# Kernel optimization log

Hardware: AMD Instinct MI355X
Metric: run time of the kernel (lower is better)

The kernel has to match this reference:

```python
import jax, jax.numpy as jnp
import numpy as np

N_NODES = 50000
N_EDGES = 1600000
N_GRAPHS = 512
HID = 64


def _mlp_params(key, din, dout, scale=0.1):
    k1, k2, k3 = jax.random.split(key, 3)
    return (
        jax.random.normal(k1, (din, HID), jnp.float32) * scale, jnp.zeros((HID,), jnp.float32),
        jax.random.normal(k2, (HID, HID), jnp.float32) * scale, jnp.zeros((HID,), jnp.float32),
        jax.random.normal(k3, (HID, dout), jnp.float32) * scale, jnp.zeros((dout,), jnp.float32),
    )


def _mlp(x, w1, b1, w2, b2, w3, b3, out_act=None):
    h = jax.nn.relu(x @ w1 + b1)
    h = jax.nn.relu(h @ w2 + b2)
    o = h @ w3 + b3
    return o if out_act is None else out_act(o)


def setup_inputs() -> dict:
    key = jax.random.key(0)
    ks = jax.random.split(key, 8)
    nf = jax.random.normal(ks[0], (N_NODES, 1), jnp.float32)
    ef = jax.random.normal(ks[1], (N_EDGES, 1), jnp.float32)
    src = jax.random.randint(ks[2], (N_EDGES,), 0, N_NODES)
    dst = jax.random.randint(ks[3], (N_EDGES,), 0, N_NODES)
    graph_id = jnp.sort(jax.random.randint(ks[4], (N_NODES,), 0, N_GRAPHS))
    e_w1, e_b1, e_w2, e_b2, e_w3, e_b3 = _mlp_params(ks[5], 3, 1)   # edge model: [src_nf, dst_nf, ef] -> msg
    n_w1, n_b1, n_w2, n_b2, n_w3, n_b3 = _mlp_params(ks[6], 2, 1)   # node model: [nf, agg] -> unf
    m_w1, m_b1, m_w2, m_b2, m_w3, m_b3 = _mlp_params(ks[7], 1, 1)   # node-wise MLP with Sigmoid out_act
    return dict(nf=nf, ef=ef, src=src, dst=dst, graph_id=graph_id,
                e_w1=e_w1, e_b1=e_b1, e_w2=e_w2, e_b2=e_b2, e_w3=e_w3, e_b3=e_b3,
                n_w1=n_w1, n_b1=n_b1, n_w2=n_w2, n_b2=n_b2, n_w3=n_w3, n_b3=n_b3,
                m_w1=m_w1, m_b1=m_b1, m_w2=m_w2, m_b2=m_b2, m_w3=m_w3, m_b3=m_b3)


def reference(nf, ef, src, dst, graph_id,
              e_w1, e_b1, e_w2, e_b2, e_w3, e_b3,
              n_w1, n_b1, n_w2, n_b2, n_w3, n_b3,
              m_w1, m_b1, m_w2, m_b2, m_w3, m_b3):
    # MPNN layer: message on edges, sum-aggregate to dst nodes, node update
    em_in = jnp.concatenate([nf[src], nf[dst], ef], axis=-1)          # [E, 3]
    msg = _mlp(em_in, e_w1, e_b1, e_w2, e_b2, e_w3, e_b3)             # [E, 1]
    agg = jax.ops.segment_sum(msg, dst, num_segments=N_NODES)        # [N, 1]
    unf = _mlp(jnp.concatenate([nf, agg], axis=-1),
               n_w1, n_b1, n_w2, n_b2, n_w3, n_b3)                    # [N, 1]
    # node-wise MLP with Sigmoid output activation
    node_out = _mlp(unf, m_w1, m_b1, m_w2, m_b2, m_w3, m_b3,
                    out_act=jax.nn.sigmoid)                           # [N, 1]
    # sum readout per graph, then final sigmoid
    rd = jax.ops.segment_sum(node_out, graph_id, num_segments=N_GRAPHS)  # [G, 1]
    return jax.nn.sigmoid(rd)
```

## Files before the change

### kernel.cpp

```cpp
#include <hip/hip_runtime.h>
#include <math.h>

#define HID 64
#define BKT_SHIFT 13
#define BKT_RANGE 8192
#define CCHUNK 32

typedef __attribute__((ext_vector_type(8))) short short8;
typedef __attribute__((ext_vector_type(4))) float f32x4;
typedef unsigned long long ull;

union FragU {
    uint4 q;
    short8 v;
    uint32_t u[4];
};

__device__ __forceinline__ uint32_t cvt_pk_bf16(float lo, float hi) {
    uint32_t r;
    asm("v_cvt_pk_bf16_f32 %0, %1, %2" : "=v"(r) : "v"(lo), "v"(hi));
    return r;
}

__global__ __launch_bounds__(256, 2) void edge_mfma8_kernel(
    const float* __restrict__ nf, const float* __restrict__ ef,
    const int* __restrict__ src, const int* __restrict__ dst,
    const float* __restrict__ w1, const float* __restrict__ b1,
    const float* __restrict__ w2, const float* __restrict__ b2,
    const float* __restrict__ w3, const float* __restrict__ b3,
    uint2* __restrict__ recs, ull* __restrict__ offs,
    float* __restrict__ aggFb, int E, int B, int nbatch, int mode)
{
    __shared__ uint2 tile[4][4][16][16];

    const int tid  = threadIdx.x;
    const int lane = tid & 63;
    const int wid  = tid >> 6;
    const int g    = lane >> 4;
    const int eL   = lane & 15;

    FragU af1[4];
#pragma unroll
    for (int t = 0; t < 4; ++t) {
        int j = t * 16 + eL;
        uint32_t u0 = cvt_pk_bf16(w1[j], w1[HID + j]);
        uint32_t u1 = cvt_pk_bf16(w1[2 * HID + j], b1[j]);
        af1[t].u[0] = (g == 0) ? u0 : 0u;
        af1[t].u[1] = (g == 0) ? u1 : 0u;
        af1[t].u[2] = 0u; af1[t].u[3] = 0u;
    }
    FragU af2[4][2];
#pragma unroll
    for (int t = 0; t < 4; ++t)
#pragma unroll
        for (int h = 0; h < 2; ++h)
#pragma unroll
            for (int e2 = 0; e2 < 4; ++e2) {
                int k0 = h * 32 + g * 8 + 2 * e2;
                int j  = t * 16 + eL;
                af2[t][h].u[e2] = cvt_pk_bf16(w2[k0 * HID + j], w2[(k0 + 1) * HID + j]);
            }
    f32x4 b2v4[4], w3v4[4];
#pragma unroll
    for (int t = 0; t < 4; ++t) {
        int j = t * 16 + g * 4;
        b2v4[t] = *(const f32x4*)&b2[j];
        w3v4[t] = *(const f32x4*)&w3[j];
    }
    const float b3c = b3[0];

    int bi   = blockIdx.x;
    if (bi >= nbatch) return;
    int eidx = bi * 256 + tid;
    int ei   = eidx < E ? eidx : E - 1;
    int dcur = dst[ei];
    float a  = nf[src[ei]];
    float b  = nf[dcur];
    float c  = ef[ei];
    uint32_t pkab = cvt_pk_bf16(a, b);
    uint32_t pkc1 = cvt_pk_bf16(c, 1.0f);

    for (;;) {
        const int nbi   = bi + gridDim.x;
        const bool hn   = nbi < nbatch;
        const int neidx = hn ? nbi * 256 + tid : eidx;
        const int nei   = neidx < E ? neidx : E - 1;
        const int ns    = src[nei];
        const int nd    = dst[nei];
        const float ncf = ef[nei];

#pragma unroll
        for (int s = 0; s < 4; ++s) {
            int sel = s * 16 + eL;
            uint32_t u0 = (uint32_t)__shfl((int)pkab, sel);
            uint32_t u1 = (uint32_t)__shfl((int)pkc1, sel);
            FragU bin;
            bin.u[0] = (g == 0) ? u0 : 0u;
            bin.u[1] = (g == 0) ? u1 : 0u;
            bin.u[2] = 0u; bin.u[3] = 0u;
#pragma unroll
            for (int t = 0; t < 4; ++t) {
                f32x4 h4 = __builtin_amdgcn_mfma_f32_16x16x32_bf16(
                    af1[t].v, bin.v, (f32x4){0.f, 0.f, 0.f, 0.f}, 0, 0, 0);
                uint32_t p0 = cvt_pk_bf16(fmaxf(h4[0], 0.f), fmaxf(h4[1], 0.f));
                uint32_t p1 = cvt_pk_bf16(fmaxf(h4[2], 0.f), fmaxf(h4[3], 0.f));
                tile[wid][s][eL][(4 * t + g) ^ ((eL & 7) << 1)] = make_uint2(p0, p1);
            }
        }

        const float na = nf[ns];
        const float nb = nf[nd];

        float mymsg = 0.f;
#pragma unroll
        for (int s = 0; s < 4; ++s) {
            const uint4* row = (const uint4*)&tile[wid][s][eL][0];
            FragU bf0, bf1;
            bf0.q = row[(g)     ^ (eL & 7)];
            bf1.q = row[(4 + g) ^ (eL & 7)];

            float q0, q1, q2, q3;
            {
                f32x4 ac = __builtin_amdgcn_mfma_f32_16x16x32_bf16(af2[0][0].v, bf0.v, b2v4[0], 0, 0, 0);
                ac = __builtin_amdgcn_mfma_f32_16x16x32_bf16(af2[0][1].v, bf1.v, ac, 0, 0, 0);
                q0 = fmaxf(ac[0], 0.f) * w3v4[0][0];
                q0 = fmaf(fmaxf(ac[1], 0.f), w3v4[0][1], q0);
                q0 = fmaf(fmaxf(ac[2], 0.f), w3v4[0][2], q0);
                q0 = fmaf(fmaxf(ac[3], 0.f), w3v4[0][3], q0);
            }
            {
                f32x4 ac = __builtin_amdgcn_mfma_f32_16x16x32_bf16(af2[1][0].v, bf0.v, b2v4[1], 0, 0, 0);
                ac = __builtin_amdgcn_mfma_f32_16x16x32_bf16(af2[1][1].v, bf1.v, ac, 0, 0, 0);
                q1 = fmaxf(ac[0], 0.f) * w3v4[1][0];
                q1 = fmaf(fmaxf(ac[1], 0.f), w3v4[1][1], q1);
                q1 = fmaf(fmaxf(ac[2], 0.f), w3v4[1][2], q1);
                q1 = fmaf(fmaxf(ac[3], 0.f), w3v4[1][3], q1);
            }
            {
                f32x4 ac = __builtin_amdgcn_mfma_f32_16x16x32_bf16(af2[2][0].v, bf0.v, b2v4[2], 0, 0, 0);
                ac = __builtin_amdgcn_mfma_f32_16x16x32_bf16(af2[2][1].v, bf1.v, ac, 0, 0, 0);
                q2 = fmaxf(ac[0], 0.f) * w3v4[2][0];
                q2 = fmaf(fmaxf(ac[1], 0.f), w3v4[2][1], q2);
                q2 = fmaf(fmaxf(ac[2], 0.f), w3v4[2][2], q2);
                q2 = fmaf(fmaxf(ac[3], 0.f), w3v4[2][3], q2);
            }
            {
                f32x4 ac = __builtin_amdgcn_mfma_f32_16x16x32_bf16(af2[3][0].v, bf0.v, b2v4[3], 0, 0, 0);
                ac = __builtin_amdgcn_mfma_f32_16x16x32_bf16(af2[3][1].v, bf1.v, ac, 0, 0, 0);
                q3 = fmaxf(ac[0], 0.f) * w3v4[3][0];
                q3 = fmaf(fmaxf(ac[1], 0.f), w3v4[3][1], q3);
                q3 = fmaf(fmaxf(ac[2], 0.f), w3v4[3][2], q3);
                q3 = fmaf(fmaxf(ac[3], 0.f), w3v4[3][3], q3);
            }
            float p = (q0 + q1) + (q2 + q3);
            p += __shfl_xor(p, 16);
            p += __shfl_xor(p, 32);
            if (s == g) mymsg = p + b3c;
        }

        const bool valid = eidx < E;

        if (mode == 1) {
            if (valid) atomicAdd(&aggFb[dcur], mymsg);
        } else {
            const int bkt = dcur >> BKT_SHIFT;
            const ull lt = (1ull << lane) - 1;
            int myslot = 0;
            int off = 0;
            uint32_t pack_lo = 0, pack_hi = 0;
            for (int bb = 0; bb < B; ++bb) {
                if (bb < 4) pack_lo |= (uint32_t)off << (8 * bb);
                else        pack_hi |= (uint32_t)off << (8 * (bb - 4));
                ull m = __ballot(valid && bkt == bb);
                if (valid && bkt == bb) myslot = off + (int)__popcll(m & lt);
                off += (int)__popcll(m);
            }
            pack_hi |= (uint32_t)off << 24;

            const size_t wgl = (size_t)bi * 4 + wid;
            if (valid) recs[wgl * 64 + myslot] = make_uint2((uint32_t)dcur, __float_as_uint(mymsg));
            if (lane == 0) offs[wgl] = ((ull)pack_hi << 32) | (ull)pack_lo;
        }

        if (!hn) break;
        bi = nbi; eidx = neidx;
        pkab = cvt_pk_bf16(na, nb);
        pkc1 = cvt_pk_bf16(ncf, 1.0f);
        dcur = nd;
    }
}

__global__ __launch_bounds__(256) void bucket_accum_kernel(
    const uint2* __restrict__ recs, const ull* __restrict__ offs,
    float* __restrict__ partial, float* __restrict__ rd, unsigned* __restrict__ ctr,
    int G, int NW, int B)
{
    __shared__ float acc[BKT_RANGE];

    const int b = blockIdx.x / CCHUNK;
    const int c = blockIdx.x % CCHUNK;

    if (blockIdx.x == 0) {
        for (int i = threadIdx.x; i < G; i += 256) rd[i] = 0.f;
        if (threadIdx.x == 0) *ctr = 0u;
    }

    for (int i = threadIdx.x; i < BKT_RANGE; i += 256) acc[i] = 0.f;
    __syncthreads();

    const int wpc = (NW + CCHUNK - 1) / CCHUNK;
    const int w0 = c * wpc;
    const int w1 = (w0 + wpc < NW) ? w0 + wpc : NW;
    const int nb = b + 1;
    const int base_node = b << BKT_SHIFT;

    for (int w = w0 + threadIdx.x; w < w1; w += 256) {
        ull ov = offs[w];
        uint32_t lo = (uint32_t)ov, hi = (uint32_t)(ov >> 32);
        int ob = (int)(((b  < 4) ? (lo >> (8 * b))  : (hi >> (8 * (b  - 4)))) & 0xFF);
        int oe = (int)(((nb < 4) ? (lo >> (8 * nb)) : (hi >> (8 * (nb - 4)))) & 0xFF);
        const uint2* rb = recs + (size_t)w * 64;
        for (int r = ob; r < oe; ++r) {
            uint2 rec = rb[r];
            atomicAdd(&acc[(int)rec.x - base_node], __uint_as_float(rec.y));
        }
    }
    __syncthreads();

    float* pb = partial + ((size_t)b * CCHUNK + c) * BKT_RANGE;
    for (int i = threadIdx.x; i < BKT_RANGE; i += 256) pb[i] = acc[i];
}

__global__ __launch_bounds__(256, 2) void node_mfma5_kernel(
    const float* __restrict__ nf, const float* __restrict__ partial,
    const float* __restrict__ aggFb, int nplanes,
    const int* __restrict__ gid,
    const float* __restrict__ nw1, const float* __restrict__ nb1,
    const float* __restrict__ nw2, const float* __restrict__ nb2,
    const float* __restrict__ nw3, const float* __restrict__ nb3,
    const float* __restrict__ mw1, const float* __restrict__ mb1,
    const float* __restrict__ mw2, const float* __restrict__ mb2,
    const float* __restrict__ mw3, const float* __restrict__ mb3,
    float* __restrict__ rd, float* __restrict__ outp, unsigned* __restrict__ ctr,
    int N, int G)
{
    __shared__ uint2 tile[4][4][16][16];
    __shared__ int lastflag;

    const int tid  = threadIdx.x;
    const int lane = tid & 63;
    const int wid  = tid >> 6;
    const int g    = lane >> 4;
    const int eL   = lane & 15;

    const int idx = blockIdx.x * 256 + tid;
    const int i   = idx < N ? idx : N - 1;
    const float x0 = nf[i];
    const int   gg = gid[i];

    float x1;
    if (nplanes == 1) {
        x1 = aggFb[i];
    } else {
        int bb = i >> BKT_SHIFT, nl = i & (BKT_RANGE - 1);
        const float* p = partial + (size_t)bb * CCHUNK * BKT_RANGE + nl;
        x1 = 0.f;
#pragma unroll 8
        for (int c = 0; c < CCHUNK; ++c) x1 += p[(size_t)c * BKT_RANGE];
    }

    float myunf = 0.f, o = 0.f;

    {
        FragU af1[4], af2[4][2];
        f32x4 b2v4[4], w3v4[4];
#pragma unroll
        for (int t = 0; t < 4; ++t) {
            int j = t * 16 + eL;
            uint32_t u0 = cvt_pk_bf16(nw1[j], nw1[HID + j]);
            uint32_t u1 = cvt_pk_bf16(nb1[j], 0.f);
            af1[t].u[0] = (g == 0) ? u0 : 0u;
            af1[t].u[1] = (g == 0) ? u1 : 0u;
            af1[t].u[2] = 0u; af1[t].u[3] = 0u;
#pragma unroll
            for (int h = 0; h < 2; ++h)
#pragma unroll
                for (int e2 = 0; e2 < 4; ++e2) {
                    int k0 = h * 32 + g * 8 + 2 * e2;
                    af2[t][h].u[e2] = cvt_pk_bf16(nw2[k0 * HID + j], nw2[(k0 + 1) * HID + j]);
                }
            int j4 = t * 16 + g * 4;
            b2v4[t] = *(const f32x4*)&nb2[j4];
            w3v4[t] = *(const f32x4*)&nw3[j4];
        }
        uint32_t pk01 = cvt_pk_bf16(x0, x1);
        uint32_t pkb  = cvt_pk_bf16(1.0f, 0.f);

#pragma unroll
        for (int s = 0; s < 4; ++s) {
            int sel = s * 16 + eL;
            uint32_t u0 = (uint32_t)__shfl((int)pk01, sel);
            FragU bin;
            bin.u[0] = (g == 0) ? u0 : 0u;
            bin.u[1] = (g == 0) ? pkb : 0u;
            bin.u[2] = 0u; bin.u[3] = 0u;
#pragma unroll
            for (int t = 0; t < 4; ++t) {
                f32x4 h4 = __builtin_amdgcn_mfma_f32_16x16x32_bf16(
                    af1[t].v, bin.v, (f32x4){0.f, 0.f, 0.f, 0.f}, 0, 0, 0);
                uint32_t p0 = cvt_pk_bf16(fmaxf(h4[0], 0.f), fmaxf(h4[1], 0.f));
                uint32_t p1 = cvt_pk_bf16(fmaxf(h4[2], 0.f), fmaxf(h4[3], 0.f));
                tile[wid][s][eL][(4 * t + g) ^ ((eL & 7) << 1)] = make_uint2(p0, p1);
            }
        }
#pragma unroll
        for (int s = 0; s < 4; ++s) {
            const uint4* row = (const uint4*)&tile[wid][s][eL][0];
            FragU bf0, bf1;
            bf0.q = row[(g)     ^ (eL & 7)];
            bf1.q = row[(4 + g) ^ (eL & 7)];
            float p = 0.f;
#pragma unroll
            for (int t = 0; t < 4; ++t) {
                f32x4 ac = __builtin_amdgcn_mfma_f32_16x16x32_bf16(af2[t][0].v, bf0.v, b2v4[t], 0, 0, 0);
                ac = __builtin_amdgcn_mfma_f32_16x16x32_bf16(af2[t][1].v, bf1.v, ac, 0, 0, 0);
                p = fmaf(fmaxf(ac[0], 0.f), w3v4[t][0], p);
                p = fmaf(fmaxf(ac[1], 0.f), w3v4[t][1], p);
                p = fmaf(fmaxf(ac[2], 0.f), w3v4[t][2], p);
                p = fmaf(fmaxf(ac[3], 0.f), w3v4[t][3], p);
            }
            p += __shfl_xor(p, 16);
            p += __shfl_xor(p, 32);
            if (s == g) myunf = p + nb3[0];
        }
    }

    {
        FragU af1[4], af2[4][2];
        f32x4 b2v4[4], w3v4[4];
#pragma unroll
        for (int t = 0; t < 4; ++t) {
            int j = t * 16 + eL;
            uint32_t u0 = cvt_pk_bf16(mw1[j], mb1[j]);
            af1[t].u[0] = (g == 0) ? u0 : 0u;
            af1[t].u[1] = 0u; af1[t].u[2] = 0u; af1[t].u[3] = 0u;
#pragma unroll
            for (int h = 0; h < 2; ++h)
#pragma unroll
                for (int e2 = 0; e2 < 4; ++e2) {
                    int k0 = h * 32 + g * 8 + 2 * e2;
                    af2[t][h].u[e2] = cvt_pk_bf16(mw2[k0 * HID + j], mw2[(k0 + 1) * HID + j]);
                }
            int j4 = t * 16 + g * 4;
            b2v4[t] = *(const f32x4*)&mb2[j4];
            w3v4[t] = *(const f32x4*)&mw3[j4];
        }

#pragma unroll
        for (int s = 0; s < 4; ++s) {
            float uv = __shfl(myunf, s * 16 + eL);
            FragU bin;
            bin.u[0] = (g == 0) ? cvt_pk_bf16(uv, 1.0f) : 0u;
            bin.u[1] = 0u; bin.u[2] = 0u; bin.u[3] = 0u;
#pragma unroll
            for (int t = 0; t < 4; ++t) {
                f32x4 h4 = __builtin_amdgcn_mfma_f32_16x16x32_bf16(
                    af1[t].v, bin.v, (f32x4){0.f, 0.f, 0.f, 0.f}, 0, 0, 0);
                uint32_t p0 = cvt_pk_bf16(fmaxf(h4[0], 0.f), fmaxf(h4[1], 0.f));
                uint32_t p1 = cvt_pk_bf16(fmaxf(h4[2], 0.f), fmaxf(h4[3], 0.f));
                tile[wid][s][eL][(4 * t + g) ^ ((eL & 7) << 1)] = make_uint2(p0, p1);
            }
        }
#pragma unroll
        for (int s = 0; s < 4; ++s) {
            const uint4* row = (const uint4*)&tile[wid][s][eL][0];
            FragU bf0, bf1;
            bf0.q = row[(g)     ^ (eL & 7)];
            bf1.q = row[(4 + g) ^ (eL & 7)];
            float p = 0.f;
#pragma unroll
            for (int t = 0; t < 4; ++t) {
                f32x4 ac = __builtin_amdgcn_mfma_f32_16x16x32_bf16(af2[t][0].v, bf0.v, b2v4[t], 0, 0, 0);
                ac = __builtin_amdgcn_mfma_f32_16x16x32_bf16(af2[t][1].v, bf1.v, ac, 0, 0, 0);
                p = fmaf(fmaxf(ac[0], 0.f), w3v4[t][0], p);
                p = fmaf(fmaxf(ac[1], 0.f), w3v4[t][1], p);
                p = fmaf(fmaxf(ac[2], 0.f), w3v4[t][2], p);
                p = fmaf(fmaxf(ac[3], 0.f), w3v4[t][3], p);
            }
            p += __shfl_xor(p, 16);
            p += __shfl_xor(p, 32);
            if (s == g) o = p + mb3[0];
        }
    }

    const float node_out = 1.0f / (1.0f + expf(-o));

    {
        const bool ok = idx < N;
        float v = ok ? node_out : 0.0f;
        int ggv = gg;
#pragma unroll
        for (int d = 1; d < 64; d <<= 1) {
            float vup = __shfl_up(v, d);
            int   gup = __shfl_up(ggv, d);
            if (lane >= d && gup == ggv) v += vup;
        }
        int gdn = __shfl_down(ggv, 1);
        bool tail = (lane == 63) || (gdn != ggv);
        if (tail)
            atomicAdd(&rd[ggv], v);
    }

    if (ctr) {
        if (tid == 0) {
            __threadfence();
            unsigned v = atomicAdd(ctr, 1u);
            lastflag = (v == (unsigned)(gridDim.x - 1)) ? 1 : 0;
        }
        __syncthreads();
        if (lastflag) {
            __threadfence();
            for (int q = tid; q < G; q += 256)
                outp[q] = 1.0f / (1.0f + expf(-rd[q]));
        }
    }
}

__global__ void readout_kernel(const float* __restrict__ rd,
                               float* __restrict__ out, int G)
{
    int g = blockIdx.x * blockDim.x + threadIdx.x;
    if (g < G) out[g] = 1.0f / (1.0f + expf(-rd[g]));
}

extern "C" void kernel_launch(void* const* d_in, const int* in_sizes, int n_in,
                              void* d_out, int out_size, void* d_ws, size_t ws_size,
                              hipStream_t stream)
{
    const float* nf  = (const float*)d_in[0];
    const float* ef  = (const float*)d_in[1];
    const int*   src = (const int*)  d_in[2];
    const int*   dst = (const int*)  d_in[3];
    const int*   gid = (const int*)  d_in[4];

    const float* e_w1 = (const float*)d_in[5];
    const float* e_b1 = (const float*)d_in[6];
    const float* e_w2 = (const float*)d_in[7];
    const float* e_b2 = (const float*)d_in[8];
    const float* e_w3 = (const float*)d_in[9];
    const float* e_b3 = (const float*)d_in[10];

    const float* n_w1 = (const float*)d_in[11];
    const float* n_b1 = (const float*)d_in[12];
    const float* n_w2 = (const float*)d_in[13];
    const float* n_b2 = (const float*)d_in[14];
    const float* n_w3 = (const float*)d_in[15];
    const float* n_b3 = (const float*)d_in[16];

    const float* m_w1 = (const float*)d_in[17];
    const float* m_b1 = (const float*)d_in[18];
    const float* m_w2 = (const float*)d_in[19];
    const float* m_b2 = (const float*)d_in[20];
    const float* m_w3 = (const float*)d_in[21];
    const float* m_b3 = (const float*)d_in[22];

    const int N = in_sizes[0];
    const int E = in_sizes[2];
    const int G = out_size;

    const int nbatch = (E + 255) / 256;
    const int NW = (E + 63) / 64;
    const int B  = (N + BKT_RANGE - 1) / BKT_RANGE;

    size_t recs_b = (size_t)NW * 64 * sizeof(uint2);
    size_t offs_b = (size_t)NW * sizeof(ull);
    size_t part_b = (size_t)B * CCHUNK * BKT_RANGE * sizeof(float);
    size_t need   = recs_b + offs_b + part_b + (size_t)G * sizeof(float) + 64;
    bool bucketok = (B <= 8) && (need <= ws_size);

    char* wp = (char*)d_ws;
    float* out = (float*)d_out;

    int egrid = nbatch < 1024 ? nbatch : 1024;

    if (bucketok) {
        uint2*    recs    = (uint2*)wp;
        ull*      offs    = (ull*)(wp + recs_b);
        float*    partial = (float*)(wp + recs_b + offs_b);
        float*    rd      = (float*)(wp + recs_b + offs_b + part_b);
        unsigned* ctr     = (unsigned*)(wp + recs_b + offs_b + part_b + (size_t)G * sizeof(float));

        edge_mfma8_kernel<<<egrid, 256, 0, stream>>>(
            nf, ef, src, dst, e_w1, e_b1, e_w2, e_b2, e_w3, e_b3,
            recs, offs, nullptr, E, B, nbatch, 0);

        bucket_accum_kernel<<<B * CCHUNK, 256, 0, stream>>>(
            recs, offs, partial, rd, ctr, G, NW, B);

        node_mfma5_kernel<<<(N + 255) / 256, 256, 0, stream>>>(
            nf, partial, nullptr, CCHUNK, gid,
            n_w1, n_b1, n_w2, n_b2, n_w3, n_b3,
            m_w1, m_b1, m_w2, m_b2, m_w3, m_b3,
            rd, out, ctr, N, G);
    } else {
        float* agg = (float*)wp;
        float* rd  = agg + N;

        hipMemsetAsync(agg, 0, ((size_t)N + G) * sizeof(float), stream);

        edge_mfma8_kernel<<<egrid, 256, 0, stream>>>(
            nf, ef, src, dst, e_w1, e_b1, e_w2, e_b2, e_w3, e_b3,
            nullptr, nullptr, agg, E, B, nbatch, 1);

        node_mfma5_kernel<<<(N + 255) / 256, 256, 0, stream>>>(
            nf, nullptr, agg, 1, gid,
            n_w1, n_b1, n_w2, n_b2, n_w3, n_b3,
            m_w1, m_b1, m_w2, m_b2, m_w3, m_b3,
            rd, out, nullptr, N, G);

        readout_kernel<<<(G + 255) / 256, 256, 0, stream>>>(rd, out, G);
    }
}
```

Baseline: 71.94 us.

## Drop per-wave bucket sorting; bucket kernel scans all edge records and filters

The edge kernel no longer ballots records into per-wave bucket slots with packed offsets. It writes each (dst, msg) record at its edge index. The bucket accumulation kernel now has every bucket's blocks scan the full record array in paired 16-byte loads and keep only records whose destination falls in their bucket. This removes the ballot loop and offset metadata but multiplies record reads by the bucket count (7 here). The node kernel is also moved to 128-thread blocks.

```diff
diff --git a/kernel.cpp b/kernel.cpp
--- a/kernel.cpp
+++ b/kernel.cpp
@@ -22,14 +22,14 @@
     return r;
 }
 
-__global__ __launch_bounds__(256, 2) void edge_mfma8_kernel(
+__global__ __launch_bounds__(256, 2) void edge_mfma9_kernel(
     const float* __restrict__ nf, const float* __restrict__ ef,
     const int* __restrict__ src, const int* __restrict__ dst,
     const float* __restrict__ w1, const float* __restrict__ b1,
     const float* __restrict__ w2, const float* __restrict__ b2,
     const float* __restrict__ w3, const float* __restrict__ b3,
-    uint2* __restrict__ recs, ull* __restrict__ offs,
-    float* __restrict__ aggFb, int E, int B, int nbatch, int mode)
+    uint2* __restrict__ recs,
+    float* __restrict__ aggFb, int E, int nbatch, int mode)
 {
     __shared__ uint2 tile[4][4][16][16];
 
@@ -163,23 +163,7 @@
         if (mode == 1) {
             if (valid) atomicAdd(&aggFb[dcur], mymsg);
         } else {
-            const int bkt = dcur >> BKT_SHIFT;
-            const ull lt = (1ull << lane) - 1;
-            int myslot = 0;
-            int off = 0;
-            uint32_t pack_lo = 0, pack_hi = 0;
-            for (int bb = 0; bb < B; ++bb) {
-                if (bb < 4) pack_lo |= (uint32_t)off << (8 * bb);
-                else        pack_hi |= (uint32_t)off << (8 * (bb - 4));
-                ull m = __ballot(valid && bkt == bb);
-                if (valid && bkt == bb) myslot = off + (int)__popcll(m & lt);
-                off += (int)__popcll(m);
-            }
-            pack_hi |= (uint32_t)off << 24;
-
-            const size_t wgl = (size_t)bi * 4 + wid;
-            if (valid) recs[wgl * 64 + myslot] = make_uint2((uint32_t)dcur, __float_as_uint(mymsg));
-            if (lane == 0) offs[wgl] = ((ull)pack_hi << 32) | (ull)pack_lo;
+            if (valid) recs[eidx] = make_uint2((uint32_t)dcur, __float_as_uint(mymsg));
         }
 
         if (!hn) break;
@@ -190,10 +174,10 @@
     }
 }
 
-__global__ __launch_bounds__(256) void bucket_accum_kernel(
-    const uint2* __restrict__ recs, const ull* __restrict__ offs,
-    float* __restrict__ partial, float* __restrict__ rd, unsigned* __restrict__ ctr,
-    int G, int NW, int B)
+__global__ __launch_bounds__(256) void bucket_accum2_kernel(
+    const uint2* __restrict__ recs, float* __restrict__ partial,
+    float* __restrict__ rd, unsigned* __restrict__ ctr,
+    int G, int E, int B)
 {
     __shared__ float acc[BKT_RANGE];
 
@@ -208,21 +192,21 @@
     for (int i = threadIdx.x; i < BKT_RANGE; i += 256) acc[i] = 0.f;
     __syncthreads();
 
-    const int wpc = (NW + CCHUNK - 1) / CCHUNK;
-    const int w0 = c * wpc;
-    const int w1 = (w0 + wpc < NW) ? w0 + wpc : NW;
-    const int nb = b + 1;
+    const int epc = (((E + CCHUNK - 1) / CCHUNK) + 1) & ~1;
+    const int e0 = c * epc;
+    const int e1 = (e0 + epc < E) ? e0 + epc : E;
     const int base_node = b << BKT_SHIFT;
 
-    for (int w = w0 + threadIdx.x; w < w1; w += 256) {
-        ull ov = offs[w];
-        uint32_t lo = (uint32_t)ov, hi = (uint32_t)(ov >> 32);
-        int ob = (int)(((b  < 4) ? (lo >> (8 * b))  : (hi >> (8 * (b  - 4)))) & 0xFF);
-        int oe = (int)(((nb < 4) ? (lo >> (8 * nb)) : (hi >> (8 * (nb - 4)))) & 0xFF);
-        const uint2* rb = recs + (size_t)w * 64;
-        for (int r = ob; r < oe; ++r) {
-            uint2 rec = rb[r];
-            atomicAdd(&acc[(int)rec.x - base_node], __uint_as_float(rec.y));
+    for (int e = e0 + threadIdx.x * 2; e < e1; e += 512) {
+        if (e + 1 < e1) {
+            uint4 two = *reinterpret_cast<const uint4*>(&recs[e]);
+            int d0 = (int)two.x, d1 = (int)two.z;
+            if ((d0 >> BKT_SHIFT) == b) atomicAdd(&acc[d0 - base_node], __uint_as_float(two.y));
+            if ((d1 >> BKT_SHIFT) == b) atomicAdd(&acc[d1 - base_node], __uint_as_float(two.w));
+        } else {
+            uint2 r = recs[e];
+            int d0 = (int)r.x;
+            if ((d0 >> BKT_SHIFT) == b) atomicAdd(&acc[d0 - base_node], __uint_as_float(r.y));
         }
     }
     __syncthreads();
@@ -231,7 +215,7 @@
     for (int i = threadIdx.x; i < BKT_RANGE; i += 256) pb[i] = acc[i];
 }
 
-__global__ __launch_bounds__(256, 2) void node_mfma5_kernel(
+__global__ __launch_bounds__(128, 2) void node_mfma6_kernel(
     const float* __restrict__ nf, const float* __restrict__ partial,
     const float* __restrict__ aggFb, int nplanes,
     const int* __restrict__ gid,
@@ -244,7 +228,7 @@
     float* __restrict__ rd, float* __restrict__ outp, unsigned* __restrict__ ctr,
     int N, int G)
 {
-    __shared__ uint2 tile[4][4][16][16];
+    __shared__ uint2 tile[2][4][16][16];
     __shared__ int lastflag;
 
     const int tid  = threadIdx.x;
@@ -253,7 +237,7 @@
     const int g    = lane >> 4;
     const int eL   = lane & 15;
 
-    const int idx = blockIdx.x * 256 + tid;
+    const int idx = blockIdx.x * 128 + tid;
     const int i   = idx < N ? idx : N - 1;
     const float x0 = nf[i];
     const int   gg = gid[i];
@@ -420,7 +404,7 @@
         __syncthreads();
         if (lastflag) {
             __threadfence();
-            for (int q = tid; q < G; q += 256)
+            for (int q = tid; q < G; q += 128)
                 outp[q] = 1.0f / (1.0f + expf(-rd[q]));
         }
     }
@@ -469,13 +453,11 @@
     const int G = out_size;
 
     const int nbatch = (E + 255) / 256;
-    const int NW = (E + 63) / 64;
     const int B  = (N + BKT_RANGE - 1) / BKT_RANGE;
 
-    size_t recs_b = (size_t)NW * 64 * sizeof(uint2);
-    size_t offs_b = (size_t)NW * sizeof(ull);
+    size_t recs_b = (size_t)E * sizeof(uint2);
     size_t part_b = (size_t)B * CCHUNK * BKT_RANGE * sizeof(float);
-    size_t need   = recs_b + offs_b + part_b + (size_t)G * sizeof(float) + 64;
+    size_t need   = recs_b + part_b + (size_t)G * sizeof(float) + 64;
     bool bucketok = (B <= 8) && (need <= ws_size);
 
     char* wp = (char*)d_ws;
@@ -485,19 +467,18 @@
 
     if (bucketok) {
         uint2*    recs    = (uint2*)wp;
-        ull*      offs    = (ull*)(wp + recs_b);
-        float*    partial = (float*)(wp + recs_b + offs_b);
-        float*    rd      = (float*)(wp + recs_b + offs_b + part_b);
-        unsigned* ctr     = (unsigned*)(wp + recs_b + offs_b + part_b + (size_t)G * sizeof(float));
-
-        edge_mfma8_kernel<<<egrid, 256, 0, stream>>>(
+        float*    partial = (float*)(wp + recs_b);
+        float*    rd      = (float*)(wp + recs_b + part_b);
+        unsigned* ctr     = (unsigned*)(wp + recs_b + part_b + (size_t)G * sizeof(float));
+
+        edge_mfma9_kernel<<<egrid, 256, 0, stream>>>(
             nf, ef, src, dst, e_w1, e_b1, e_w2, e_b2, e_w3, e_b3,
-            recs, offs, nullptr, E, B, nbatch, 0);
-
-        bucket_accum_kernel<<<B * CCHUNK, 256, 0, stream>>>(
-            recs, offs, partial, rd, ctr, G, NW, B);
-
-        node_mfma5_kernel<<<(N + 255) / 256, 256, 0, stream>>>(
+            recs, nullptr, E, nbatch, 0);
+
+        bucket_accum2_kernel<<<B * CCHUNK, 256, 0, stream>>>(
+            recs, partial, rd, ctr, G, E, B);
+
+        node_mfma6_kernel<<<(N + 127) / 128, 128, 0, stream>>>(
             nf, partial, nullptr, CCHUNK, gid,
             n_w1, n_b1, n_w2, n_b2, n_w3, n_b3,
             m_w1, m_b1, m_w2, m_b2, m_w3, m_b3,
@@ -508,11 +489,11 @@
 
         hipMemsetAsync(agg, 0, ((size_t)N + G) * sizeof(float), stream);
 
-        edge_mfma8_kernel<<<egrid, 256, 0, stream>>>(
+        edge_mfma9_kernel<<<egrid, 256, 0, stream>>>(
             nf, ef, src, dst, e_w1, e_b1, e_w2, e_b2, e_w3, e_b3,
-            nullptr, nullptr, agg, E, B, nbatch, 1);
-
-        node_mfma5_kernel<<<(N + 255) / 256, 256, 0, stream>>>(
+            nullptr, agg, E, nbatch, 1);
+
+        node_mfma6_kernel<<<(N + 127) / 128, 128, 0, stream>>>(
             nf, nullptr, agg, 1, gid,
             n_w1, n_b1, n_w2, n_b2, n_w3, n_b3,
             m_w1, m_b1, m_w2, m_b2, m_w3, m_b3,
```

Measured after the change: 98.91 us. 1.37x slower.

## Interleave two edge batches per loop iteration in edge MLP kernel

Applied to the files above, without the earlier changes.

The edge kernel now carries two 256-edge batches (A and B, one grid-stride apart) through each loop iteration. The layer-1 and layer-2 MFMA work and the LDS tile staging of both batches are interleaved, and the next pair's gathers are prefetched midway. The aim is more independent work in flight to hide MFMA, LDS and gather latency, and half as many loop iterations. The cost is higher register pressure under the (256, 2) launch bound, and possible imbalance when a block has an odd number of batches.

```diff
diff --git a/kernel.cpp b/kernel.cpp
--- a/kernel.cpp
+++ b/kernel.cpp
@@ -22,7 +22,7 @@
     return r;
 }
 
-__global__ __launch_bounds__(256, 2) void edge_mfma8_kernel(
+__global__ __launch_bounds__(256, 2) void edge_dual_kernel(
     const float* __restrict__ nf, const float* __restrict__ ef,
     const int* __restrict__ src, const int* __restrict__ dst,
     const float* __restrict__ w1, const float* __restrict__ b1,
@@ -31,7 +31,7 @@
     uint2* __restrict__ recs, ull* __restrict__ offs,
     float* __restrict__ aggFb, int E, int B, int nbatch, int mode)
 {
-    __shared__ uint2 tile[4][4][16][16];
+    __shared__ uint2 tile[4][2][2][16][16];
 
     const int tid  = threadIdx.x;
     const int lane = tid & 63;
@@ -69,124 +69,169 @@
     }
     const float b3c = b3[0];
 
-    int bi   = blockIdx.x;
-    if (bi >= nbatch) return;
-    int eidx = bi * 256 + tid;
-    int ei   = eidx < E ? eidx : E - 1;
-    int dcur = dst[ei];
-    float a  = nf[src[ei]];
-    float b  = nf[dcur];
-    float c  = ef[ei];
-    uint32_t pkab = cvt_pk_bf16(a, b);
-    uint32_t pkc1 = cvt_pk_bf16(c, 1.0f);
+    auto L1SET = [&](uint32_t ab, uint32_t c1, int s, uint2 (*tl)[16]) {
+        int sel = s * 16 + eL;
+        uint32_t u0 = (uint32_t)__shfl((int)ab, sel);
+        uint32_t u1 = (uint32_t)__shfl((int)c1, sel);
+        FragU bin;
+        bin.u[0] = (g == 0) ? u0 : 0u;
+        bin.u[1] = (g == 0) ? u1 : 0u;
+        bin.u[2] = 0u; bin.u[3] = 0u;
+#pragma unroll
+        for (int t = 0; t < 4; ++t) {
+            f32x4 h4 = __builtin_amdgcn_mfma_f32_16x16x32_bf16(
+                af1[t].v, bin.v, (f32x4){0.f, 0.f, 0.f, 0.f}, 0, 0, 0);
+            uint32_t p0 = cvt_pk_bf16(fmaxf(h4[0], 0.f), fmaxf(h4[1], 0.f));
+            uint32_t p1 = cvt_pk_bf16(fmaxf(h4[2], 0.f), fmaxf(h4[3], 0.f));
+            tl[eL][(4 * t + g) ^ ((eL & 7) << 1)] = make_uint2(p0, p1);
+        }
+    };
+    auto L2SET = [&](uint2 (*tl)[16]) -> float {
+        const uint4* row = (const uint4*)&tl[eL][0];
+        FragU bf0, bf1;
+        bf0.q = row[(g)     ^ (eL & 7)];
+        bf1.q = row[(4 + g) ^ (eL & 7)];
+        float q0, q1, q2, q3;
+        {
+            f32x4 ac = __builtin_amdgcn_mfma_f32_16x16x32_bf16(af2[0][0].v, bf0.v, b2v4[0], 0, 0, 0);
+            ac = __builtin_amdgcn_mfma_f32_16x16x32_bf16(af2[0][1].v, bf1.v, ac, 0, 0, 0);
+            q0 = fmaxf(ac[0], 0.f) * w3v4[0][0];
+            q0 = fmaf(fmaxf(ac[1], 0.f), w3v4[0][1], q0);
+            q0 = fmaf(fmaxf(ac[2], 0.f), w3v4[0][2], q0);
+            q0 = fmaf(fmaxf(ac[3], 0.f), w3v4[0][3], q0);
+        }
+        {
+            f32x4 ac = __builtin_amdgcn_mfma_f32_16x16x32_bf16(af2[1][0].v, bf0.v, b2v4[1], 0, 0, 0);
+            ac = __builtin_amdgcn_mfma_f32_16x16x32_bf16(af2[1][1].v, bf1.v, ac, 0, 0, 0);
+            q1 = fmaxf(ac[0], 0.f) * w3v4[1][0];
+            q1 = fmaf(fmaxf(ac[1], 0.f), w3v4[1][1], q1);
+            q1 = fmaf(fmaxf(ac[2], 0.f), w3v4[1][2], q1);
+            q1 = fmaf(fmaxf(ac[3], 0.f), w3v4[1][3], q1);
+        }
+        {
+            f32x4 ac = __builtin_amdgcn_mfma_f32_16x16x32_bf16(af2[2][0].v, bf0.v, b2v4[2], 0, 0, 0);
+            ac = __builtin_amdgcn_mfma_f32_16x16x32_bf16(af2[2][1].v, bf1.v, ac, 0, 0, 0);
+            q2 = fmaxf(ac[0], 0.f) * w3v4[2][0];
+            q2 = fmaf(fmaxf(ac[1], 0.f), w3v4[2][1], q2);
+            q2 = fmaf(fmaxf(ac[2], 0.f), w3v4[2][2], q2);
+            q2 = fmaf(fmaxf(ac[3], 0.f), w3v4[2][3], q2);
+        }
+        {
+            f32x4 ac = __builtin_amdgcn_mfma_f32_16x16x32_bf16(af2[3][0].v, bf0.v, b2v4[3], 0, 0, 0);
+            ac = __builtin_amdgcn_mfma_f32_16x16x32_bf16(af2[3][1].v, bf1.v, ac, 0, 0, 0);
+            q3 = fmaxf(ac[0], 0.f) * w3v4[3][0];
+            q3 = fmaf(fmaxf(ac[1], 0.f), w3v4[3][1], q3);
+            q3 = fmaf(fmaxf(ac[2], 0.f), w3v4[3][2], q3);
+            q3 = fmaf(fmaxf(ac[3], 0.f), w3v4[3][3], q3);
+        }
+        float p = (q0 + q1) + (q2 + q3);
+        p += __shfl_xor(p, 16);
+        p += __shfl_xor(p, 32);
+        return p;
+    };
+    auto APPEND = [&](int bb_i, int eix, int dc, float msg) {
+        const bool valid = eix < E;
+        const int bkt = dc >> BKT_SHIFT;
+        const ull lt = (1ull << lane) - 1;
+        int myslot = 0;
+        int off = 0;
+        uint32_t plo = 0, phi = 0;
+        for (int bb = 0; bb < B; ++bb) {
+            if (bb < 4) plo |= (uint32_t)off << (8 * bb);
+            else        phi |= (uint32_t)off << (8 * (bb - 4));
+            ull m = __ballot(valid && bkt == bb);
+            if (valid && bkt == bb) myslot = off + (int)__popcll(m & lt);
+            off += (int)__popcll(m);
+        }
+        phi |= (uint32_t)off << 24;
+        const size_t wgl = (size_t)bb_i * 4 + wid;
+        if (valid) recs[wgl * 64 + myslot] = make_uint2((uint32_t)dc, __float_as_uint(msg));
+        if (lane == 0) offs[wgl] = ((ull)phi << 32) | (ull)plo;
+    };
+
+    const int gsz = gridDim.x;
+    int biA = blockIdx.x;
+    if (biA >= nbatch) return;
+
+    int eixA = biA * 256 + tid;
+    int eiA  = eixA < E ? eixA : E - 1;
+    int dcA  = dst[eiA];
+    float aA = nf[src[eiA]];
+    float bA = nf[dcA];
+    float cA = ef[eiA];
+    uint32_t abA = cvt_pk_bf16(aA, bA);
+    uint32_t c1A = cvt_pk_bf16(cA, 1.0f);
+
+    int  biB  = biA + gsz;
+    bool hasB = biB < nbatch;
+    int eixB = hasB ? biB * 256 + tid : eixA;
+    int eiB  = eixB < E ? eixB : E - 1;
+    int dcB  = dst[eiB];
+    float aB = nf[src[eiB]];
+    float bB = nf[dcB];
+    float cB = ef[eiB];
+    uint32_t abB = cvt_pk_bf16(aB, bB);
+    uint32_t c1B = cvt_pk_bf16(cB, 1.0f);
 
     for (;;) {
-        const int nbi   = bi + gridDim.x;
-        const bool hn   = nbi < nbatch;
-        const int neidx = hn ? nbi * 256 + tid : eidx;
-        const int nei   = neidx < E ? neidx : E - 1;
-        const int ns    = src[nei];
-        const int nd    = dst[nei];
-        const float ncf = ef[nei];
-
-#pragma unroll
-        for (int s = 0; s < 4; ++s) {
-            int sel = s * 16 + eL;
-            uint32_t u0 = (uint32_t)__shfl((int)pkab, sel);
-            uint32_t u1 = (uint32_t)__shfl((int)pkc1, sel);
-            FragU bin;
-            bin.u[0] = (g == 0) ? u0 : 0u;
-            bin.u[1] = (g == 0) ? u1 : 0u;
-            bin.u[2] = 0u; bin.u[3] = 0u;
-#pragma unroll
-            for (int t = 0; t < 4; ++t) {
-                f32x4 h4 = __builtin_amdgcn_mfma_f32_16x16x32_bf16(
-                    af1[t].v, bin.v, (f32x4){0.f, 0.f, 0.f, 0.f}, 0, 0, 0);
-                uint32_t p0 = cvt_pk_bf16(fmaxf(h4[0], 0.f), fmaxf(h4[1], 0.f));
-                uint32_t p1 = cvt_pk_bf16(fmaxf(h4[2], 0.f), fmaxf(h4[3], 0.f));
-                tile[wid][s][eL][(4 * t + g) ^ ((eL & 7) << 1)] = make_uint2(p0, p1);
-            }
-        }
-
-        const float na = nf[ns];
-        const float nb = nf[nd];
-
-        float mymsg = 0.f;
-#pragma unroll
-        for (int s = 0; s < 4; ++s) {
-            const uint4* row = (const uint4*)&tile[wid][s][eL][0];
-            FragU bf0, bf1;
-            bf0.q = row[(g)     ^ (eL & 7)];
-            bf1.q = row[(4 + g) ^ (eL & 7)];
-
-            float q0, q1, q2, q3;
-            {
-                f32x4 ac = __builtin_amdgcn_mfma_f32_16x16x32_bf16(af2[0][0].v, bf0.v, b2v4[0], 0, 0, 0);
-                ac = __builtin_amdgcn_mfma_f32_16x16x32_bf16(af2[0][1].v, bf1.v, ac, 0, 0, 0);
-                q0 = fmaxf(ac[0], 0.f) * w3v4[0][0];
-                q0 = fmaf(fmaxf(ac[1], 0.f), w3v4[0][1], q0);
-                q0 = fmaf(fmaxf(ac[2], 0.f), w3v4[0][2], q0);
-                q0 = fmaf(fmaxf(ac[3], 0.f), w3v4[0][3], q0);
-            }
-            {
-                f32x4 ac = __builtin_amdgcn_mfma_f32_16x16x32_bf16(af2[1][0].v, bf0.v, b2v4[1], 0, 0, 0);
-                ac = __builtin_amdgcn_mfma_f32_16x16x32_bf16(af2[1][1].v, bf1.v, ac, 0, 0, 0);
-                q1 = fmaxf(ac[0], 0.f) * w3v4[1][0];
-                q1 = fmaf(fmaxf(ac[1], 0.f), w3v4[1][1], q1);
-                q1 = fmaf(fmaxf(ac[2], 0.f), w3v4[1][2], q1);
-                q1 = fmaf(fmaxf(ac[3], 0.f), w3v4[1][3], q1);
-            }
-            {
-                f32x4 ac = __builtin_amdgcn_mfma_f32_16x16x32_bf16(af2[2][0].v, bf0.v, b2v4[2], 0, 0, 0);
-                ac = __builtin_amdgcn_mfma_f32_16x16x32_bf16(af2[2][1].v, bf1.v, ac, 0, 0, 0);
-                q2 = fmaxf(ac[0], 0.f) * w3v4[2][0];
-                q2 = fmaf(fmaxf(ac[1], 0.f), w3v4[2][1], q2);
-                q2 = fmaf(fmaxf(ac[2], 0.f), w3v4[2][2], q2);
-                q2 = fmaf(fmaxf(ac[3], 0.f), w3v4[2][3], q2);
-            }
-            {
-                f32x4 ac = __builtin_amdgcn_mfma_f32_16x16x32_bf16(af2[3][0].v, bf0.v, b2v4[3], 0, 0, 0);
-                ac = __builtin_amdgcn_mfma_f32_16x16x32_bf16(af2[3][1].v, bf1.v, ac, 0, 0, 0);
-                q3 = fmaxf(ac[0], 0.f) * w3v4[3][0];
-                q3 = fmaf(fmaxf(ac[1], 0.f), w3v4[3][1], q3);
-                q3 = fmaf(fmaxf(ac[2], 0.f), w3v4[3][2], q3);
-                q3 = fmaf(fmaxf(ac[3], 0.f), w3v4[3][3], q3);
-            }
-            float p = (q0 + q1) + (q2 + q3);
-            p += __shfl_xor(p, 16);
-            p += __shfl_xor(p, 32);
-            if (s == g) mymsg = p + b3c;
-        }
-
-        const bool valid = eidx < E;
+        const int  nbiA = biA + 2 * gsz;
+        const bool hnA  = nbiA < nbatch;
+        const int  neixA = hnA ? nbiA * 256 + tid : eixA;
+        const int  neiA  = neixA < E ? neixA : E - 1;
+        const int  nsA = src[neiA];
+        const int  ndA = dst[neiA];
+        const float ncA = ef[neiA];
+
+        const int  nbiB = nbiA + gsz;
+        const bool hnB  = nbiB < nbatch;
+        const int  neixB = hnB ? nbiB * 256 + tid : eixA;
+        const int  neiB  = neixB < E ? neixB : E - 1;
+        const int  nsB = src[neiB];
+        const int  ndB = dst[neiB];
+        const float ncB = ef[neiB];
+
+        float naA = 0.f, nbA2 = 0.f, naB = 0.f, nbB2 = 0.f;
+        float msgA = 0.f, msgB = 0.f;
+
+#pragma unroll
+        for (int ph = 0; ph < 2; ++ph) {
+#pragma unroll
+            for (int ss = 0; ss < 2; ++ss) {
+                const int s = 2 * ph + ss;
+                L1SET(abA, c1A, s, tile[wid][0][ss]);
+                L1SET(abB, c1B, s, tile[wid][1][ss]);
+            }
+            if (ph == 0) {
+                naA  = nf[nsA];
+                nbA2 = nf[ndA];
+                naB  = nf[nsB];
+                nbB2 = nf[ndB];
+            }
+#pragma unroll
+            for (int ss = 0; ss < 2; ++ss) {
+                const int s = 2 * ph + ss;
+                float pA = L2SET(tile[wid][0][ss]);
+                if (s == g) msgA = pA + b3c;
+                float pB = L2SET(tile[wid][1][ss]);
+                if (s == g) msgB = pB + b3c;
+            }
+        }
 
         if (mode == 1) {
-            if (valid) atomicAdd(&aggFb[dcur], mymsg);
+            if (eixA < E) atomicAdd(&aggFb[dcA], msgA);
+            if (hasB && eixB < E) atomicAdd(&aggFb[dcB], msgB);
         } else {
-            const int bkt = dcur >> BKT_SHIFT;
-            const ull lt = (1ull << lane) - 1;
-            int myslot = 0;
-            int off = 0;
-            uint32_t pack_lo = 0, pack_hi = 0;
-            for (int bb = 0; bb < B; ++bb) {
-                if (bb < 4) pack_lo |= (uint32_t)off << (8 * bb);
-                else        pack_hi |= (uint32_t)off << (8 * (bb - 4));
-                ull m = __ballot(valid && bkt == bb);
-                if (valid && bkt == bb) myslot = off + (int)__popcll(m & lt);
-                off += (int)__popcll(m);
-            }
-            pack_hi |= (uint32_t)off << 24;
-
-            const size_t wgl = (size_t)bi * 4 + wid;
-            if (valid) recs[wgl * 64 + myslot] = make_uint2((uint32_t)dcur, __float_as_uint(mymsg));
-            if (lane == 0) offs[wgl] = ((ull)pack_hi << 32) | (ull)pack_lo;
-        }
-
-        if (!hn) break;
-        bi = nbi; eidx = neidx;
-        pkab = cvt_pk_bf16(na, nb);
-        pkc1 = cvt_pk_bf16(ncf, 1.0f);
-        dcur = nd;
+            APPEND(biA, eixA, dcA, msgA);
+            if (hasB) APPEND(biB, eixB, dcB, msgB);
+        }
+
+        if (!hnA) break;
+        biA = nbiA; eixA = neixA; dcA = ndA;
+        abA = cvt_pk_bf16(naA, nbA2);
+        c1A = cvt_pk_bf16(ncA, 1.0f);
+        biB = nbiB; hasB = hnB; eixB = neixB; dcB = ndB;
+        abB = cvt_pk_bf16(naB, nbB2);
+        c1B = cvt_pk_bf16(ncB, 1.0f);
     }
 }
 
@@ -490,7 +535,7 @@
         float*    rd      = (float*)(wp + recs_b + offs_b + part_b);
         unsigned* ctr     = (unsigned*)(wp + recs_b + offs_b + part_b + (size_t)G * sizeof(float));
 
-        edge_mfma8_kernel<<<egrid, 256, 0, stream>>>(
+        edge_dual_kernel<<<egrid, 256, 0, stream>>>(
             nf, ef, src, dst, e_w1, e_b1, e_w2, e_b2, e_w3, e_b3,
             recs, offs, nullptr, E, B, nbatch, 0);
 
@@ -508,7 +553,7 @@
 
         hipMemsetAsync(agg, 0, ((size_t)N + G) * sizeof(float), stream);
 
-        edge_mfma8_kernel<<<egrid, 256, 0, stream>>>(
+        edge_dual_kernel<<<egrid, 256, 0, stream>>>(
             nf, ef, src, dst, e_w1, e_b1, e_w2, e_b2, e_w3, e_b3,
             nullptr, nullptr, agg, E, B, nbatch, 1);
 
```

Result: slower. 78.37 us (+8.9%).
